# Kernel tuning notes

Hardware: AMD Instinct MI355X
Metric: run time of the kernel (lower is better)

Reference implementation:

```python
import jax, jax.numpy as jnp
import numpy as np

N = 100_000      # nodes
E = 1_600_000    # edges
B = 256          # graphs
DIM = 64
EPS = 1e-5


def _batchnorm(h, gamma, beta):
    # BatchNorm1d in training mode: batch mean, biased variance
    mu = jnp.mean(h, axis=0)
    var = jnp.mean((h - mu) ** 2, axis=0)
    return (h - mu) * jax.lax.rsqrt(var + EPS) * gamma + beta


def setup_inputs() -> dict:
    key = jax.random.key(0)
    ks = jax.random.split(key, 12)
    x = jax.random.normal(ks[0], (N, DIM), dtype=jnp.float32)
    edge_index = jax.random.randint(ks[1], (2, E), 0, N, dtype=jnp.int64)
    edge_attr = jax.random.normal(ks[2], (E, DIM), dtype=jnp.float32)
    state = jax.random.normal(ks[3], (B, DIM), dtype=jnp.float32)
    batch = jnp.sort(jax.random.randint(ks[4], (N,), 0, B, dtype=jnp.int64))
    s = 0.05
    params = {
        "W1": jax.random.normal(ks[5], (DIM, 3 * DIM), dtype=jnp.float32) * s,
        "b1": jnp.zeros((DIM,), jnp.float32),
        "g1": jnp.ones((DIM,), jnp.float32),
        "be1": jnp.zeros((DIM,), jnp.float32),
        "W2": jax.random.normal(ks[6], (DIM, DIM), dtype=jnp.float32) * s,
        "b2": jnp.zeros((DIM,), jnp.float32),
        "g2": jnp.ones((DIM,), jnp.float32),
        "be2": jnp.zeros((DIM,), jnp.float32),
        "W3": jax.random.normal(ks[7], (DIM, DIM), dtype=jnp.float32) * s,
        "b3": jnp.zeros((DIM,), jnp.float32),
        "g3": jnp.ones((DIM,), jnp.float32),
        "be3": jnp.zeros((DIM,), jnp.float32),
    }
    return {"x": x, "edge_index": edge_index, "edge_attr": edge_attr,
            "state": state, "batch": batch, **params}


def reference(x, edge_index, edge_attr, state, batch,
              W1, b1, g1, be1, W2, b2, g2, be2, W3, b3, g3, be3):
    n = x.shape[0]
    src = edge_index[0]
    # scatter-mean of edge_attr onto destination-of-src nodes
    sums = jax.ops.segment_sum(edge_attr, src, num_segments=n)
    cnt = jax.ops.segment_sum(jnp.ones((edge_attr.shape[0],), edge_attr.dtype),
                              src, num_segments=n)
    v_mean = sums / jnp.maximum(cnt, 1.0)[:, None]
    comb = jnp.concatenate([x, v_mean, state[batch]], axis=1)  # [N, 3*DIM]
    h = jax.nn.relu(comb @ W1.T + b1)
    h = _batchnorm(h, g1, be1)
    h = jax.nn.relu(h @ W2.T + b2)
    h = _batchnorm(h, g2, be2)
    h = h @ W3.T + b3
    return _batchnorm(h, g3, be3)
```

## Files before the change

### kernel.cpp

```cpp
#include <hip/hip_runtime.h>

#define NN 100000
#define NE 1600000
#define EPSV 1e-5f
#define NTILE 1563

typedef float f32x4 __attribute__((ext_vector_type(4)));
typedef short s16x8 __attribute__((ext_vector_type(8)));

__device__ __forceinline__ unsigned short f2bf(float f) {
  unsigned int u = __float_as_uint(f);
  u += 0x7fffu + ((u >> 16) & 1u);
  return (unsigned short)(u >> 16);
}

__device__ __forceinline__ float bf2f(unsigned short s) {
  return __uint_as_float(((unsigned int)s) << 16);
}

__device__ __forceinline__ ushort4 pack4(float4 v) {
  ushort4 s;
  s.x = f2bf(v.x); s.y = f2bf(v.y); s.z = f2bf(v.z); s.w = f2bf(v.w);
  return s;
}

__global__ __launch_bounds__(256) void k_bucket_g1a(
    const int* __restrict__ ei, int* __restrict__ cnt, int* __restrict__ eids,
    const float4* __restrict__ x4, const float4* __restrict__ state4,
    const int* __restrict__ batch, const float4* __restrict__ w14,
    f32x4* __restrict__ ph) {
  __shared__ unsigned short lx[64][136];
  __shared__ unsigned short lw[64][136];
  const int idx = blockIdx.x;
  const int tid = threadIdx.x;
  const bool is_g1a = ((idx % 5) == 2) && (idx / 5 < NTILE);
  if (!is_g1a) {
    int nga = idx / 5 + (((idx % 5) > 2) ? 1 : 0);
    if (nga > NTILE) nga = NTILE;
    int e = (idx - nga) * 256 + tid;
    int src = ei[e];
    int pos = atomicAdd(&cnt[src], 1);
    if (pos < 64) eids[(size_t)src * 64 + pos] = e;
    return;
  }
  const int tile = idx / 5;
  const int nodeBase = tile * 64;
#pragma unroll
  for (int i = 0; i < 4; ++i) {
    int t = tid + i * 256;
    int j = t >> 4, q = t & 15;
    *(ushort4*)&lw[j][q * 4]      = pack4(w14[j * 48 + q]);
    *(ushort4*)&lw[j][64 + q * 4] = pack4(w14[j * 48 + 32 + q]);
  }
#pragma unroll
  for (int i = 0; i < 4; ++i) {
    int t = tid + i * 256;
    int node = t >> 4, q = t & 15;
    int g = nodeBase + node;
    float4 vx = {0,0,0,0}, vs = {0,0,0,0};
    if (g < NN) {
      vx = x4[(size_t)g * 16 + q];
      vs = state4[batch[g] * 16 + q];
    }
    *(ushort4*)&lx[node][q * 4]      = pack4(vx);
    *(ushort4*)&lx[node][64 + q * 4] = pack4(vs);
  }
  __syncthreads();
  const int lane = tid & 63, w = tid >> 6;
  const int rg = lane >> 4, ci = lane & 15;
  f32x4 acc[4] = {{0,0,0,0},{0,0,0,0},{0,0,0,0},{0,0,0,0}};
#pragma unroll
  for (int s = 0; s < 4; ++s) {
    int k0 = 32 * s + rg * 8;
    s16x8 a = *(const s16x8*)&lx[w * 16 + ci][k0];
#pragma unroll
    for (int c = 0; c < 4; ++c) {
      s16x8 b = *(const s16x8*)&lw[c * 16 + ci][k0];
      acc[c] = __builtin_amdgcn_mfma_f32_16x16x32_bf16(a, b, acc[c], 0, 0, 0);
    }
  }
#pragma unroll
  for (int c = 0; c < 4; ++c)
    ph[(size_t)tile * 1024 + tid * 4 + c] = acc[c];
}

__global__ __launch_bounds__(256) void k_gather_g1b(
    const int* __restrict__ cnt, const int* __restrict__ eids,
    const float4* __restrict__ ea4,
    const float4* __restrict__ w14, const float* __restrict__ b1,
    const f32x4* __restrict__ ph, unsigned short* __restrict__ h1,
    float* __restrict__ Sout, float* __restrict__ Qout) {
  __shared__ unsigned short lv[64][72];
  __shared__ unsigned short lwv[64][72];
  __shared__ float ssum[64], ssq[64];
  const int tid = threadIdx.x;
  const int tile = blockIdx.x;
  const int nodeBase = tile * 64;
  if (tid < 64) { ssum[tid] = 0.f; ssq[tid] = 0.f; }
#pragma unroll
  for (int i = 0; i < 4; ++i) {
    int t = tid + i * 256;
    int j = t >> 4, q = t & 15;
    *(ushort4*)&lwv[j][q * 4] = pack4(w14[j * 48 + 16 + q]);
  }
  const int lane = tid & 63, w = tid >> 6;
  const int grp = lane >> 4, q = lane & 15;
  for (int k = 0; k < 16; ++k) {
    int n = nodeBase + w * 16 + k;
    float ax = 0.f, ay = 0.f, az = 0.f, aw = 0.f;
    int c = 0;
    if (n < NN) {
      const int* elist = eids + (size_t)n * 64;
      c = cnt[n];
      int m = c < 64 ? c : 64;
      int rm = m - 1;
      {
        int r0 = grp,      r1 = 4 + grp,  r2 = 8 + grp,  r3 = 12 + grp;
        int r4 = 16 + grp, r5 = 20 + grp, r6 = 24 + grp, r7 = 28 + grp;
        int i0 = elist[r0 < m ? r0 : rm];
        int i1 = elist[r1 < m ? r1 : rm];
        int i2 = elist[r2 < m ? r2 : rm];
        int i3 = elist[r3 < m ? r3 : rm];
        int i4 = elist[r4 < m ? r4 : rm];
        int i5 = elist[r5 < m ? r5 : rm];
        int i6 = elist[r6 < m ? r6 : rm];
        int i7 = elist[r7 < m ? r7 : rm];
        float4 v0 = ea4[(size_t)i0 * 16 + q];
        float4 v1 = ea4[(size_t)i1 * 16 + q];
        float4 v2 = ea4[(size_t)i2 * 16 + q];
        float4 v3 = ea4[(size_t)i3 * 16 + q];
        float4 v4 = ea4[(size_t)i4 * 16 + q];
        float4 v5 = ea4[(size_t)i5 * 16 + q];
        float4 v6 = ea4[(size_t)i6 * 16 + q];
        float4 v7 = ea4[(size_t)i7 * 16 + q];
        float m0 = r0 < m ? 1.f : 0.f, m1 = r1 < m ? 1.f : 0.f;
        float m2 = r2 < m ? 1.f : 0.f, m3 = r3 < m ? 1.f : 0.f;
        ax += m0 * v0.x + m1 * v1.x + m2 * v2.x + m3 * v3.x;
        ay += m0 * v0.y + m1 * v1.y + m2 * v2.y + m3 * v3.y;
        az += m0 * v0.z + m1 * v1.z + m2 * v2.z + m3 * v3.z;
        aw += m0 * v0.w + m1 * v1.w + m2 * v2.w + m3 * v3.w;
        float m4 = r4 < m ? 1.f : 0.f, m5 = r5 < m ? 1.f : 0.f;
        float m6 = r6 < m ? 1.f : 0.f, m7 = r7 < m ? 1.f : 0.f;
        ax += m4 * v4.x + m5 * v5.x + m6 * v6.x + m7 * v7.x;
        ay += m4 * v4.y + m5 * v5.y + m6 * v6.y + m7 * v7.y;
        az += m4 * v4.z + m5 * v5.z + m6 * v6.z + m7 * v7.z;
        aw += m4 * v4.w + m5 * v5.w + m6 * v6.w + m7 * v7.w;
      }
      if (m > 32) {
        for (int e = 32; e < m; e += 16) {
          int r0 = e + grp, r1 = e + 4 + grp, r2 = e + 8 + grp, r3 = e + 12 + grp;
          int i0 = elist[r0 < m ? r0 : rm];
          int i1 = elist[r1 < m ? r1 : rm];
          int i2 = elist[r2 < m ? r2 : rm];
          int i3 = elist[r3 < m ? r3 : rm];
          float4 v0 = ea4[(size_t)i0 * 16 + q];
          float4 v1 = ea4[(size_t)i1 * 16 + q];
          float4 v2 = ea4[(size_t)i2 * 16 + q];
          float4 v3 = ea4[(size_t)i3 * 16 + q];
          float m0 = r0 < m ? 1.f : 0.f, m1 = r1 < m ? 1.f : 0.f;
          float m2 = r2 < m ? 1.f : 0.f, m3 = r3 < m ? 1.f : 0.f;
          ax += m0 * v0.x + m1 * v1.x + m2 * v2.x + m3 * v3.x;
          ay += m0 * v0.y + m1 * v1.y + m2 * v2.y + m3 * v3.y;
          az += m0 * v0.z + m1 * v1.z + m2 * v2.z + m3 * v3.z;
          aw += m0 * v0.w + m1 * v1.w + m2 * v2.w + m3 * v3.w;
        }
      }
    }
    ax += __shfl_xor(ax, 16); ay += __shfl_xor(ay, 16);
    az += __shfl_xor(az, 16); aw += __shfl_xor(aw, 16);
    ax += __shfl_xor(ax, 32); ay += __shfl_xor(ay, 32);
    az += __shfl_xor(az, 32); aw += __shfl_xor(aw, 32);
    if (lane < 16) {
      float inv = 1.0f / fmaxf((float)c, 1.0f);
      float4 r; r.x = ax * inv; r.y = ay * inv; r.z = az * inv; r.w = aw * inv;
      *(ushort4*)&lv[w * 16 + k][lane * 4] = pack4(r);
    }
  }
  __syncthreads();
  const int rg = lane >> 4, ci = lane & 15;
  f32x4 acc[4];
#pragma unroll
  for (int cc = 0; cc < 4; ++cc) acc[cc] = ph[(size_t)tile * 1024 + tid * 4 + cc];
#pragma unroll
  for (int s = 0; s < 2; ++s) {
    int k0 = 32 * s + rg * 8;
    s16x8 a = *(const s16x8*)&lv[w * 16 + ci][k0];
#pragma unroll
    for (int cc = 0; cc < 4; ++cc) {
      s16x8 b = *(const s16x8*)&lwv[cc * 16 + ci][k0];
      acc[cc] = __builtin_amdgcn_mfma_f32_16x16x32_bf16(a, b, acc[cc], 0, 0, 0);
    }
  }
  __syncthreads();
  unsigned short (*lo)[72] = (unsigned short(*)[72])lwv;
#pragma unroll
  for (int cc = 0; cc < 4; ++cc) {
    int col = cc * 16 + ci;
    float bb = b1[col];
    float ls = 0.f, lq = 0.f;
#pragma unroll
    for (int r = 0; r < 4; ++r) {
      int row = w * 16 + rg * 4 + r;
      float v = fmaxf(acc[cc][r] + bb, 0.f);
      lo[row][col] = f2bf(v);
      if (nodeBase + row < NN) { ls += v; lq += v * v; }
    }
    atomicAdd(&ssum[col], ls);
    atomicAdd(&ssq[col], lq);
  }
  __syncthreads();
#pragma unroll
  for (int i = 0; i < 2; ++i) {
    int t = tid + i * 256;
    int row = t >> 3, q2 = t & 7;
    int g = nodeBase + row;
    if (g < NN) *(s16x8*)&h1[(size_t)g * 64 + q2 * 8] = *(const s16x8*)&lo[row][q2 * 8];
  }
  if (tid < 64) {
    unsafeAtomicAdd(&Sout[tid], ssum[tid]);
    unsafeAtomicAdd(&Qout[tid], ssq[tid]);
  }
}

template <bool RELU>
__global__ __launch_bounds__(256) void k_gemm64f(
    const s16x8* __restrict__ A8,
    const float* __restrict__ Wf,
    const float* __restrict__ bias,
    const float* __restrict__ gm, const float* __restrict__ bt,
    const float* __restrict__ Sin, const float* __restrict__ Qin,
    unsigned short* __restrict__ Obf,
    float* __restrict__ Sout, float* __restrict__ Qout) {
  __shared__ unsigned short la[64][72];
  __shared__ unsigned short lwf[64][72];
  __shared__ float lA[64], lC[64], ld[64], red[256], ssum[64], ssq[64];
  const int tid = threadIdx.x;
  const int nodeBase = blockIdx.x * 64;
  if (tid < 64) {
    float mu = Sin[tid] * (1.0f / NN);
    float var = Qin[tid] * (1.0f / NN) - mu * mu;
    float a = gm[tid] * rsqrtf(var + EPSV);
    lA[tid] = a; lC[tid] = bt[tid] - mu * a;
    ssum[tid] = 0.f; ssq[tid] = 0.f;
  }
  __syncthreads();
#pragma unroll
  for (int i = 0; i < 2; ++i) {
    int t = tid + i * 256;
    int row = t >> 3, q = t & 7;
    int g = nodeBase + row;
    s16x8 v = {};
    if (g < NN) v = A8[(size_t)g * 8 + q];
    *(s16x8*)&la[row][q * 8] = v;
  }
#pragma unroll
  for (int i = 0; i < 16; ++i) {
    int t = tid + i * 256;
    lwf[t >> 6][t & 63] = f2bf(Wf[t] * lA[t & 63]);
  }
  {
    int j = tid >> 2, p = tid & 3;
    const float* Wr = Wf + j * 64 + p * 16;
    float s = 0.f;
#pragma unroll
    for (int k = 0; k < 16; ++k) s += lC[p * 16 + k] * Wr[k];
    red[tid] = s;
  }
  __syncthreads();
  if (tid < 64) ld[tid] = bias[tid] + red[tid*4] + red[tid*4+1] + red[tid*4+2] + red[tid*4+3];
  __syncthreads();
  const int lane = tid & 63, w = tid >> 6;
  const int rg = lane >> 4, ci = lane & 15;
  f32x4 acc[4] = {{0,0,0,0},{0,0,0,0},{0,0,0,0},{0,0,0,0}};
#pragma unroll
  for (int s = 0; s < 2; ++s) {
    int k0 = 32 * s + rg * 8;
    s16x8 a = *(const s16x8*)&la[w * 16 + ci][k0];
#pragma unroll
    for (int c = 0; c < 4; ++c) {
      s16x8 b = *(const s16x8*)&lwf[c * 16 + ci][k0];
      acc[c] = __builtin_amdgcn_mfma_f32_16x16x32_bf16(a, b, acc[c], 0, 0, 0);
    }
  }
  __syncthreads();
  unsigned short (*lo)[72] = (unsigned short(*)[72])la;
#pragma unroll
  for (int c = 0; c < 4; ++c) {
    int col = c * 16 + ci;
    float dd = ld[col];
    float ls = 0.f, lq = 0.f;
#pragma unroll
    for (int r = 0; r < 4; ++r) {
      int row = w * 16 + rg * 4 + r;
      float v = acc[c][r] + dd;
      if (RELU) v = fmaxf(v, 0.f);
      lo[row][col] = f2bf(v);
      if (nodeBase + row < NN) { ls += v; lq += v * v; }
    }
    atomicAdd(&ssum[col], ls);
    atomicAdd(&ssq[col], lq);
  }
  __syncthreads();
#pragma unroll
  for (int i = 0; i < 2; ++i) {
    int t = tid + i * 256;
    int row = t >> 3, q = t & 7;
    int g = nodeBase + row;
    if (g < NN) *(s16x8*)&Obf[(size_t)g * 64 + q * 8] = *(const s16x8*)&lo[row][q * 8];
  }
  if (tid < 64) {
    unsafeAtomicAdd(&Sout[tid], ssum[tid]);
    unsafeAtomicAdd(&Qout[tid], ssq[tid]);
  }
}

__global__ __launch_bounds__(256) void k_bn3(
    const s16x8* __restrict__ h3b, const float* __restrict__ gm,
    const float* __restrict__ bt, const float* __restrict__ S,
    const float* __restrict__ Q, float4* __restrict__ out) {
  __shared__ float lA[64], lC[64];
  const int tid = threadIdx.x;
  if (tid < 64) {
    float mu = S[tid] * (1.0f / NN);
    float var = Q[tid] * (1.0f / NN) - mu * mu;
    float a = gm[tid] * rsqrtf(var + EPSV);
    lA[tid] = a;
    lC[tid] = bt[tid] - mu * a;
  }
  __syncthreads();
  const int total = NN * 8;
  for (int idx = blockIdx.x * 256 + tid; idx < total; idx += gridDim.x * 256) {
    s16x8 v = h3b[idx];
    int k = (idx & 7) * 8;
    float4 o0, o1;
    o0.x = bf2f((unsigned short)v[0]) * lA[k]     + lC[k];
    o0.y = bf2f((unsigned short)v[1]) * lA[k + 1] + lC[k + 1];
    o0.z = bf2f((unsigned short)v[2]) * lA[k + 2] + lC[k + 2];
    o0.w = bf2f((unsigned short)v[3]) * lA[k + 3] + lC[k + 3];
    o1.x = bf2f((unsigned short)v[4]) * lA[k + 4] + lC[k + 4];
    o1.y = bf2f((unsigned short)v[5]) * lA[k + 5] + lC[k + 5];
    o1.z = bf2f((unsigned short)v[6]) * lA[k + 6] + lC[k + 6];
    o1.w = bf2f((unsigned short)v[7]) * lA[k + 7] + lC[k + 7];
    out[idx * 2]     = o0;
    out[idx * 2 + 1] = o1;
  }
}

extern "C" void kernel_launch(void* const* d_in, const int* in_sizes, int n_in,
                              void* d_out, int out_size, void* d_ws, size_t ws_size,
                              hipStream_t stream) {
  const float* x     = (const float*)d_in[0];
  const int*   ei    = (const int*)d_in[1];
  const float* ea    = (const float*)d_in[2];
  const float* state = (const float*)d_in[3];
  const int*   batch = (const int*)d_in[4];
  const float* W1  = (const float*)d_in[5];
  const float* b1  = (const float*)d_in[6];
  const float* g1  = (const float*)d_in[7];
  const float* be1 = (const float*)d_in[8];
  const float* W2  = (const float*)d_in[9];
  const float* b2  = (const float*)d_in[10];
  const float* g2  = (const float*)d_in[11];
  const float* be2 = (const float*)d_in[12];
  const float* W3  = (const float*)d_in[13];
  const float* b3  = (const float*)d_in[14];
  const float* g3  = (const float*)d_in[15];
  const float* be3 = (const float*)d_in[16];

  char* ws = (char*)d_ws;
  int*   cnt  = (int*)ws;
  float* S1   = (float*)(ws + 400000);
  float* Q1 = S1 + 64;
  float* S2 = S1 + 128;
  float* Q2 = S1 + 192;
  float* S3 = S1 + 256;
  float* Q3 = S1 + 320;
  int*            eids = (int*)(ws + 401536);
  unsigned short* h3b  = (unsigned short*)(ws + 401536);
  unsigned short* h2   = (unsigned short*)(ws + 26018432);
  unsigned short* h1   = (unsigned short*)(ws + 38818432);
  f32x4*          ph   = (f32x4*)(ws + 51618432);

  hipMemsetAsync(ws, 0, 401536, stream);

  k_bucket_g1a<<<6250 + NTILE, 256, 0, stream>>>(
      ei, cnt, eids, (const float4*)x, (const float4*)state, batch,
      (const float4*)W1, ph);
  k_gather_g1b<<<NTILE, 256, 0, stream>>>(cnt, eids, (const float4*)ea,
                                          (const float4*)W1, b1, ph, h1, S1, Q1);
  k_gemm64f<true><<<NTILE, 256, 0, stream>>>(
      (const s16x8*)h1, W2, b2, g1, be1, S1, Q1, h2, S2, Q2);
  k_gemm64f<false><<<NTILE, 256, 0, stream>>>(
      (const s16x8*)h2, W3, b3, g2, be2, S2, Q2, h3b, S3, Q3);
  k_bn3<<<2048, 256, 0, stream>>>((const s16x8*)h3b, g3, be3, S3, Q3, (float4*)d_out);
}
```

Before: 343.1 us.

## Fuse tail GEMMs and batchnorms into one cooperative kernel with grid syncs

Replaces the three tail kernels (GEMM2+BN stats, GEMM3+BN stats, final BN apply) with one cooperative kernel of 512 blocks. Each block keeps its 3-4 node tiles of activations resident in LDS across stages and uses grid.sync to wait for global BN statistics. This removes the h2/h3 round-trips through global memory and two kernel launches. In exchange the kernel carries a large LDS footprint, runs at limited occupancy, and pays for two grid-wide barriers. If the cooperative launch fails it falls back to the old kernels.

```diff
diff --git a/kernel.cpp b/kernel.cpp
--- a/kernel.cpp
+++ b/kernel.cpp
@@ -1,9 +1,13 @@
 #include <hip/hip_runtime.h>
+#include <hip/hip_cooperative_groups.h>
+
+namespace cg = cooperative_groups;
 
 #define NN 100000
 #define NE 1600000
 #define EPSV 1e-5f
 #define NTILE 1563
+#define TGRID 512
 
 typedef float f32x4 __attribute__((ext_vector_type(4)));
 typedef short s16x8 __attribute__((ext_vector_type(8)));
@@ -222,10 +226,201 @@
   }
 }
 
+struct TailArgs {
+  const s16x8* h1;
+  const float *W2, *b2, *g1, *be1;
+  const float *W3, *b3, *g2, *be2;
+  const float *g3, *be3;
+  float *S1, *Q1, *S2, *Q2, *S3, *Q3;
+  float4* out4;
+};
+
+__global__ __launch_bounds__(256, 2) void k_tail(TailArgs A) {
+  __shared__ unsigned short ht[4][64][72];
+  __shared__ unsigned short lwf[64][72];
+  __shared__ float lA[64], lC[64], ld[64], red[256], ssum[64], ssq[64];
+  cg::grid_group grid = cg::this_grid();
+  const int tid = threadIdx.x;
+  const int b = blockIdx.x;
+  const int lane = tid & 63, w = tid >> 6;
+  const int rg = lane >> 4, ci = lane & 15;
+  const int nt = (b + 3 * TGRID < NTILE) ? 4 : 3;
+
+  for (int t = 0; t < nt; ++t) {
+    int nodeBase = (b + t * TGRID) * 64;
+#pragma unroll
+    for (int i = 0; i < 2; ++i) {
+      int tt = tid + i * 256;
+      int row = tt >> 3, q = tt & 7;
+      int g = nodeBase + row;
+      s16x8 v = {};
+      if (g < NN) v = A.h1[(size_t)g * 8 + q];
+      *(s16x8*)&ht[t][row][q * 8] = v;
+    }
+  }
+
+  {
+    if (tid < 64) {
+      float mu = A.S1[tid] * (1.0f / NN);
+      float var = A.Q1[tid] * (1.0f / NN) - mu * mu;
+      float a = A.g1[tid] * rsqrtf(var + EPSV);
+      lA[tid] = a; lC[tid] = A.be1[tid] - mu * a;
+      ssum[tid] = 0.f; ssq[tid] = 0.f;
+    }
+    __syncthreads();
+#pragma unroll
+    for (int i = 0; i < 16; ++i) {
+      int tt = tid + i * 256;
+      lwf[tt >> 6][tt & 63] = f2bf(A.W2[tt] * lA[tt & 63]);
+    }
+    {
+      int j = tid >> 2, p = tid & 3;
+      const float* Wr = A.W2 + j * 64 + p * 16;
+      float s = 0.f;
+#pragma unroll
+      for (int k = 0; k < 16; ++k) s += lC[p * 16 + k] * Wr[k];
+      red[tid] = s;
+    }
+    __syncthreads();
+    if (tid < 64) ld[tid] = A.b2[tid] + red[tid*4] + red[tid*4+1] + red[tid*4+2] + red[tid*4+3];
+    __syncthreads();
+    for (int t = 0; t < nt; ++t) {
+      int nodeBase = (b + t * TGRID) * 64;
+      f32x4 acc[4] = {{0,0,0,0},{0,0,0,0},{0,0,0,0},{0,0,0,0}};
+#pragma unroll
+      for (int s = 0; s < 2; ++s) {
+        int k0 = 32 * s + rg * 8;
+        s16x8 a = *(const s16x8*)&ht[t][w * 16 + ci][k0];
+#pragma unroll
+        for (int c = 0; c < 4; ++c) {
+          s16x8 bb = *(const s16x8*)&lwf[c * 16 + ci][k0];
+          acc[c] = __builtin_amdgcn_mfma_f32_16x16x32_bf16(a, bb, acc[c], 0, 0, 0);
+        }
+      }
+#pragma unroll
+      for (int c = 0; c < 4; ++c) {
+        int col = c * 16 + ci;
+        float dd = ld[col];
+        float ls = 0.f, lq = 0.f;
+#pragma unroll
+        for (int r = 0; r < 4; ++r) {
+          int row = w * 16 + rg * 4 + r;
+          float v = fmaxf(acc[c][r] + dd, 0.f);
+          ht[t][row][col] = f2bf(v);
+          if (nodeBase + row < NN) { ls += v; lq += v * v; }
+        }
+        atomicAdd(&ssum[col], ls);
+        atomicAdd(&ssq[col], lq);
+      }
+    }
+    __syncthreads();
+    if (tid < 64) {
+      unsafeAtomicAdd(&A.S2[tid], ssum[tid]);
+      unsafeAtomicAdd(&A.Q2[tid], ssq[tid]);
+    }
+    __threadfence();
+  }
+  grid.sync();
+
+  {
+    if (tid < 64) {
+      float Sv = atomicAdd(&A.S2[tid], 0.0f);
+      float Qv = atomicAdd(&A.Q2[tid], 0.0f);
+      float mu = Sv * (1.0f / NN);
+      float var = Qv * (1.0f / NN) - mu * mu;
+      float a = A.g2[tid] * rsqrtf(var + EPSV);
+      lA[tid] = a; lC[tid] = A.be2[tid] - mu * a;
+      ssum[tid] = 0.f; ssq[tid] = 0.f;
+    }
+    __syncthreads();
+#pragma unroll
+    for (int i = 0; i < 16; ++i) {
+      int tt = tid + i * 256;
+      lwf[tt >> 6][tt & 63] = f2bf(A.W3[tt] * lA[tt & 63]);
+    }
+    {
+      int j = tid >> 2, p = tid & 3;
+      const float* Wr = A.W3 + j * 64 + p * 16;
+      float s = 0.f;
+#pragma unroll
+      for (int k = 0; k < 16; ++k) s += lC[p * 16 + k] * Wr[k];
+      red[tid] = s;
+    }
+    __syncthreads();
+    if (tid < 64) ld[tid] = A.b3[tid] + red[tid*4] + red[tid*4+1] + red[tid*4+2] + red[tid*4+3];
+    __syncthreads();
+    for (int t = 0; t < nt; ++t) {
+      int nodeBase = (b + t * TGRID) * 64;
+      f32x4 acc[4] = {{0,0,0,0},{0,0,0,0},{0,0,0,0},{0,0,0,0}};
+#pragma unroll
+      for (int s = 0; s < 2; ++s) {
+        int k0 = 32 * s + rg * 8;
+        s16x8 a = *(const s16x8*)&ht[t][w * 16 + ci][k0];
+#pragma unroll
+        for (int c = 0; c < 4; ++c) {
+          s16x8 bb = *(const s16x8*)&lwf[c * 16 + ci][k0];
+          acc[c] = __builtin_amdgcn_mfma_f32_16x16x32_bf16(a, bb, acc[c], 0, 0, 0);
+        }
+      }
+#pragma unroll
+      for (int c = 0; c < 4; ++c) {
+        int col = c * 16 + ci;
+        float dd = ld[col];
+        float ls = 0.f, lq = 0.f;
+#pragma unroll
+        for (int r = 0; r < 4; ++r) {
+          int row = w * 16 + rg * 4 + r;
+          float v = acc[c][r] + dd;
+          ht[t][row][col] = f2bf(v);
+          if (nodeBase + row < NN) { ls += v; lq += v * v; }
+        }
+        atomicAdd(&ssum[col], ls);
+        atomicAdd(&ssq[col], lq);
+      }
+    }
+    __syncthreads();
+    if (tid < 64) {
+      unsafeAtomicAdd(&A.S3[tid], ssum[tid]);
+      unsafeAtomicAdd(&A.Q3[tid], ssq[tid]);
+    }
+    __threadfence();
+  }
+  grid.sync();
+
+  {
+    if (tid < 64) {
+      float Sv = atomicAdd(&A.S3[tid], 0.0f);
+      float Qv = atomicAdd(&A.Q3[tid], 0.0f);
+      float mu = Sv * (1.0f / NN);
+      float var = Qv * (1.0f / NN) - mu * mu;
+      float a = A.g3[tid] * rsqrtf(var + EPSV);
+      lA[tid] = a; lC[tid] = A.be3[tid] - mu * a;
+    }
+    __syncthreads();
+    for (int t = 0; t < nt; ++t) {
+      int nodeBase = (b + t * TGRID) * 64;
+#pragma unroll
+      for (int i = 0; i < 4; ++i) {
+        int idx = tid + i * 256;
+        int row = idx >> 4, q = idx & 15;
+        int g = nodeBase + row;
+        if (g < NN) {
+          int k = q * 4;
+          float4 o;
+          o.x = bf2f(ht[t][row][k])     * lA[k]     + lC[k];
+          o.y = bf2f(ht[t][row][k + 1]) * lA[k + 1] + lC[k + 1];
+          o.z = bf2f(ht[t][row][k + 2]) * lA[k + 2] + lC[k + 2];
+          o.w = bf2f(ht[t][row][k + 3]) * lA[k + 3] + lC[k + 3];
+          A.out4[(size_t)g * 16 + q] = o;
+        }
+      }
+    }
+  }
+}
+
 template <bool RELU>
 __global__ __launch_bounds__(256) void k_gemm64f(
-    const s16x8* __restrict__ A8,
-    const float* __restrict__ Wf,
+    const s16x8* __restrict__ A8, const float* __restrict__ Wf,
     const float* __restrict__ bias,
     const float* __restrict__ gm, const float* __restrict__ bt,
     const float* __restrict__ Sin, const float* __restrict__ Qin,
@@ -354,18 +549,6 @@
   const float* ea    = (const float*)d_in[2];
   const float* state = (const float*)d_in[3];
   const int*   batch = (const int*)d_in[4];
-  const float* W1  = (const float*)d_in[5];
-  const float* b1  = (const float*)d_in[6];
-  const float* g1  = (const float*)d_in[7];
-  const float* be1 = (const float*)d_in[8];
-  const float* W2  = (const float*)d_in[9];
-  const float* b2  = (const float*)d_in[10];
-  const float* g2  = (const float*)d_in[11];
-  const float* be2 = (const float*)d_in[12];
-  const float* W3  = (const float*)d_in[13];
-  const float* b3  = (const float*)d_in[14];
-  const float* g3  = (const float*)d_in[15];
-  const float* be3 = (const float*)d_in[16];
 
   char* ws = (char*)d_ws;
   int*   cnt  = (int*)ws;
@@ -376,21 +559,39 @@
   float* S3 = S1 + 256;
   float* Q3 = S1 + 320;
   int*            eids = (int*)(ws + 401536);
-  unsigned short* h3b  = (unsigned short*)(ws + 401536);
-  unsigned short* h2   = (unsigned short*)(ws + 26018432);
-  unsigned short* h1   = (unsigned short*)(ws + 38818432);
-  f32x4*          ph   = (f32x4*)(ws + 51618432);
+  unsigned short* h1   = (unsigned short*)(ws + 26018432);
+  f32x4*          ph   = (f32x4*)(ws + 38818432);
+  unsigned short* h2   = (unsigned short*)(ws + 64418432);
+  unsigned short* h3b  = (unsigned short*)(ws + 77218432);
 
   hipMemsetAsync(ws, 0, 401536, stream);
 
   k_bucket_g1a<<<6250 + NTILE, 256, 0, stream>>>(
       ei, cnt, eids, (const float4*)x, (const float4*)state, batch,
-      (const float4*)W1, ph);
+      (const float4*)d_in[5], ph);
   k_gather_g1b<<<NTILE, 256, 0, stream>>>(cnt, eids, (const float4*)ea,
-                                          (const float4*)W1, b1, ph, h1, S1, Q1);
-  k_gemm64f<true><<<NTILE, 256, 0, stream>>>(
-      (const s16x8*)h1, W2, b2, g1, be1, S1, Q1, h2, S2, Q2);
-  k_gemm64f<false><<<NTILE, 256, 0, stream>>>(
-      (const s16x8*)h2, W3, b3, g2, be2, S2, Q2, h3b, S3, Q3);
-  k_bn3<<<2048, 256, 0, stream>>>((const s16x8*)h3b, g3, be3, S3, Q3, (float4*)d_out);
-}
+                                          (const float4*)d_in[5],
+                                          (const float*)d_in[6], ph, h1, S1, Q1);
+  TailArgs ta;
+  ta.h1 = (const s16x8*)h1;
+  ta.W2 = (const float*)d_in[9];  ta.b2 = (const float*)d_in[10];
+  ta.g1 = (const float*)d_in[7];  ta.be1 = (const float*)d_in[8];
+  ta.W3 = (const float*)d_in[13]; ta.b3 = (const float*)d_in[14];
+  ta.g2 = (const float*)d_in[11]; ta.be2 = (const float*)d_in[12];
+  ta.g3 = (const float*)d_in[15]; ta.be3 = (const float*)d_in[16];
+  ta.S1 = S1; ta.Q1 = Q1; ta.S2 = S2; ta.Q2 = Q2; ta.S3 = S3; ta.Q3 = Q3;
+  ta.out4 = (float4*)d_out;
+  void* kargs[] = {&ta};
+  hipError_t rc = hipLaunchCooperativeKernel((const void*)k_tail, dim3(TGRID),
+                                             dim3(256), kargs, 0u, stream);
+  if (rc != hipSuccess) {
+    k_gemm64f<true><<<NTILE, 256, 0, stream>>>(
+        (const s16x8*)h1, (const float*)d_in[9], (const float*)d_in[10],
+        (const float*)d_in[7], (const float*)d_in[8], S1, Q1, h2, S2, Q2);
+    k_gemm64f<false><<<NTILE, 256, 0, stream>>>(
+        (const s16x8*)h2, (const float*)d_in[13], (const float*)d_in[14],
+        (const float*)d_in[11], (const float*)d_in[12], S2, Q2, h3b, S3, Q3);
+    k_bn3<<<2048, 256, 0, stream>>>((const s16x8*)h3b, (const float*)d_in[15],
+                                    (const float*)d_in[16], S3, Q3, (float4*)d_out);
+  }
+}
```

New measurement: 470.1 us. +37.0%, slower.
